# Optimization experiments

Hardware: AMD Instinct MI355X
Metric: run time of the kernel (lower is better)

Reference implementation:

```python
import jax, jax.numpy as jnp
import numpy as np

NUM_CLASSES = 80
L_BOX, L_OBJ, L_CLS = 5.0, 1.0, 1.0


def setup_inputs() -> dict:
    key = jax.random.key(0)
    k0, k1, k2, k3, k4 = jax.random.split(key, 5)
    B, N = 32, 50
    C = 5 + NUM_CLASSES
    pred0 = jax.random.normal(k0, (B, C, 64, 64), dtype=jnp.float32)
    pred1 = jax.random.normal(k1, (B, C, 32, 32), dtype=jnp.float32)
    pred2 = jax.random.normal(k2, (B, C, 16, 16), dtype=jnp.float32)
    # normalized cxcywh in (0,1)
    boxes = jax.random.uniform(k3, (B, N, 4), dtype=jnp.float32, minval=0.01, maxval=0.99)
    labels = jax.random.randint(k4, (B, N), 0, NUM_CLASSES, dtype=jnp.int32)
    return {"pred0": pred0, "pred1": pred1, "pred2": pred2, "boxes": boxes, "labels": labels}


def _bce_with_logits_mean(x, t):
    # numerically stable BCEWithLogits, mean reduction
    return jnp.mean(jnp.maximum(x, 0.0) - x * t + jnp.log1p(jnp.exp(-jnp.abs(x))))


def _build_targets(boxes, labels, b, h, w):
    # boxes: [B,N,4] normalized cxcywh; labels: [B,N]
    B, N, _ = boxes.shape
    bi = jnp.repeat(jnp.arange(B), N)            # [B*N]
    bf = boxes.reshape(-1, 4)                    # [B*N,4]
    lf = labels.reshape(-1)                      # [B*N]
    gx = bf[:, 0] * w
    gy = bf[:, 1] * h
    gi = jnp.minimum(gx.astype(jnp.int32), w - 1)  # int() truncation; gx >= 0
    gj = jnp.minimum(gy.astype(jnp.int32), h - 1)
    obj_t = jnp.zeros((b, 1, h, w), jnp.float32).at[bi, 0, gj, gi].set(1.0)
    vals = jnp.stack([gx - gi, gy - gj, bf[:, 2], bf[:, 3]], axis=1)  # [B*N,4]
    ch4 = jnp.arange(4)
    box_t = jnp.zeros((b, 4, h, w), jnp.float32).at[
        bi[:, None], ch4[None, :], gj[:, None], gi[:, None]].set(vals)
    cls_t = jnp.zeros((b, NUM_CLASSES, h, w), jnp.float32).at[bi, lf, gj, gi].set(1.0)
    return box_t, obj_t, cls_t


def _scale_loss(pred, boxes, labels):
    b, _, h, w = pred.shape
    box_t, obj_t, cls_t = _build_targets(boxes, labels, b, h, w)
    pb = jnp.clip(pred[:, :4], -10.0, 10.0)
    po = jnp.clip(pred[:, 4:5], -10.0, 10.0)
    pc = jnp.clip(pred[:, 5:], -10.0, 10.0)
    box_loss = jnp.mean((pb - box_t) ** 2)
    obj_loss = _bce_with_logits_mean(po, obj_t)
    cls_loss = _bce_with_logits_mean(pc, cls_t)
    # torch code zeroes non-finite losses; clamped logits keep these finite,
    # mirrored with jnp.where for faithfulness
    box_loss = jnp.where(jnp.isfinite(box_loss), box_loss, 0.0)
    obj_loss = jnp.where(jnp.isfinite(obj_loss), obj_loss, 0.0)
    cls_loss = jnp.where(jnp.isfinite(cls_loss), cls_loss, 0.0)
    return L_BOX * box_loss + L_OBJ * obj_loss + L_CLS * cls_loss


def reference(pred0, pred1, pred2, boxes, labels):
    total = (_scale_loss(pred0, boxes, labels)
             + _scale_loss(pred1, boxes, labels)
             + _scale_loss(pred2, boxes, labels))
    return jnp.clip(total / 3.0, 0.0, 1000000.0)
```

## Files before the change

kernel.cpp:

```cpp
#include <hip/hip_runtime.h>
#include <math.h>

#define NCLS 80
#define BB   32
#define NBOX 50
#define CC   85

#define GRID1 2048
#define BLK1  256

__device__ __forceinline__ float clip10(float x) {
    return fminf(fmaxf(x, -10.f), 10.f);
}

__device__ __forceinline__ float bce0(float x) {
    return fmaxf(x, 0.f) + __logf(1.f + __expf(-fabsf(x)));
}

__global__ __launch_bounds__(BLK1) void base_kernel(
    const float* __restrict__ p0, const float* __restrict__ p1,
    const float* __restrict__ p2,
    const float* __restrict__ boxes, const int* __restrict__ labels,
    double* __restrict__ partial)
{
    const int tid = blockIdx.x * BLK1 + threadIdx.x;
    const int nth = GRID1 * BLK1;
    const float* ps[3] = {p0, p1, p2};
    const int hw4s[3]  = {64*64/4, 32*32/4, 16*16/4};

    float part[9];
    #pragma unroll
    for (int s = 0; s < 3; ++s) {
        const float4* p = (const float4*)ps[s];
        const int hw4 = hw4s[s];
        const int n4  = BB * CC * hw4;
        float bx = 0.f, ob = 0.f, cl = 0.f;
        for (int i = tid; i < n4; i += nth) {
            float4 v = p[i];
            int c = (i / hw4) % CC;
            float a0 = clip10(v.x), a1 = clip10(v.y);
            float a2 = clip10(v.z), a3 = clip10(v.w);
            if (c < 4) {
                bx += a0*a0 + a1*a1 + a2*a2 + a3*a3;
            } else if (c == 4) {
                ob += bce0(a0) + bce0(a1) + bce0(a2) + bce0(a3);
            } else {
                cl += bce0(a0) + bce0(a1) + bce0(a2) + bce0(a3);
            }
        }
        part[3*s+0] = bx; part[3*s+1] = ob; part[3*s+2] = cl;
    }

    __shared__ int   s_cell[NBOX];
    __shared__ int   s_lab[NBOX];
    __shared__ float s_vx[NBOX], s_vy[NBOX], s_vw[NBOX], s_vh[NBOX];

    const bool doCorr = (blockIdx.x < 3 * BB);
    const int  cs = blockIdx.x / BB;
    const int  cb = blockIdx.x % BB;
    const int  Ws[3] = {64, 32, 16};

    if (doCorr && threadIdx.x < 64) {
        const int n = threadIdx.x;
        const int W = Ws[cs];
        if (n < NBOX) {
            const float* bp = boxes + ((size_t)cb * NBOX + n) * 4;
            float gx = bp[0] * (float)W;
            float gy = bp[1] * (float)W;
            int gi = min((int)gx, W - 1);
            int gj = min((int)gy, W - 1);
            s_cell[n] = gj * W + gi;
            s_lab[n]  = labels[cb * NBOX + n];
            s_vx[n] = gx - (float)gi;
            s_vy[n] = gy - (float)gj;
            s_vw[n] = bp[2];
            s_vh[n] = bp[3];
        }
    }
    __syncthreads();
    if (doCorr && threadIdx.x < 64) {
        const int n = threadIdx.x;
        const int W = Ws[cs], hw = W * W;
        const float* pred = ps[cs];
        float cbx = 0.f, cob = 0.f, ccl = 0.f;
        if (n < NBOX) {
            const int cell = s_cell[n], lab = s_lab[n];
            bool lastCell = true, lastCls = true;
            for (int m = n + 1; m < NBOX; ++m) {
                if (s_cell[m] == cell) {
                    lastCell = false;
                    if (s_lab[m] == lab) lastCls = false;
                }
            }
            const float* pb_base = pred + (size_t)(cb * CC) * hw + cell;
            if (lastCell) {
                float vals[4] = {s_vx[n], s_vy[n], s_vw[n], s_vh[n]};
                #pragma unroll
                for (int c = 0; c < 4; ++c) {
                    float pb = clip10(pb_base[c * hw]);
                    float d  = pb - vals[c];
                    cbx += d * d - pb * pb;
                }
                float po = clip10(pb_base[4 * hw]);
                cob -= po;
            }
            if (lastCls) {
                float pc = clip10(pb_base[(5 + lab) * hw]);
                ccl -= pc;
            }
        }
        #pragma unroll
        for (int off = 32; off > 0; off >>= 1) {
            cbx += __shfl_down(cbx, off);
            cob += __shfl_down(cob, off);
            ccl += __shfl_down(ccl, off);
        }
        if (n == 0) {
            part[3*cs+0] += cbx;
            part[3*cs+1] += cob;
            part[3*cs+2] += ccl;
        }
    }

    #pragma unroll
    for (int k = 0; k < 9; ++k) {
        float v = part[k];
        #pragma unroll
        for (int off = 32; off > 0; off >>= 1) v += __shfl_down(v, off);
        part[k] = v;
    }
    __shared__ float sred[BLK1/64][9];
    const int wave = threadIdx.x >> 6;
    const int lane = threadIdx.x & 63;
    if (lane == 0) {
        #pragma unroll
        for (int k = 0; k < 9; ++k) sred[wave][k] = part[k];
    }
    __syncthreads();
    if (threadIdx.x == 0) {
        double* o = partial + (size_t)blockIdx.x * 9;
        #pragma unroll
        for (int k = 0; k < 9; ++k)
            o[k] = (double)(sred[0][k] + sred[1][k] + sred[2][k] + sred[3][k]);
    }
}

__global__ __launch_bounds__(256) void final_kernel(
    const double* __restrict__ partial, float* __restrict__ out, int nb)
{
    double loc[9];
    #pragma unroll
    for (int k = 0; k < 9; ++k) loc[k] = 0.0;
    for (int i = threadIdx.x; i < nb; i += 256) {
        const double* row = partial + (size_t)i * 9;
        #pragma unroll
        for (int k = 0; k < 9; ++k) loc[k] += row[k];
    }
    #pragma unroll
    for (int k = 0; k < 9; ++k) {
        double v = loc[k];
        #pragma unroll
        for (int off = 32; off > 0; off >>= 1) v += __shfl_down(v, off);
        loc[k] = v;
    }
    __shared__ double sred[4][9];
    const int wave = threadIdx.x >> 6;
    const int lane = threadIdx.x & 63;
    if (lane == 0) {
        #pragma unroll
        for (int k = 0; k < 9; ++k) sred[wave][k] = loc[k];
    }
    __syncthreads();
    if (threadIdx.x == 0) {
        const double hws[3] = {4096.0, 1024.0, 256.0};
        double total = 0.0;
        #pragma unroll
        for (int s = 0; s < 3; ++s) {
            double hw  = hws[s];
            double tb = sred[0][3*s+0] + sred[1][3*s+0] + sred[2][3*s+0] + sred[3][3*s+0];
            double to = sred[0][3*s+1] + sred[1][3*s+1] + sred[2][3*s+1] + sred[3][3*s+1];
            double tc = sred[0][3*s+2] + sred[1][3*s+2] + sred[2][3*s+2] + sred[3][3*s+2];
            double box = tb / (32.0 * 4.0 * hw);
            double ob  = to / (32.0 * hw);
            double cl  = tc / (32.0 * 80.0 * hw);
            total += 5.0 * box + ob + cl;
        }
        total /= 3.0;
        total = fmin(fmax(total, 0.0), 1000000.0);
        out[0] = (float)total;
    }
}

extern "C" void kernel_launch(void* const* d_in, const int* in_sizes, int n_in,
                              void* d_out, int out_size, void* d_ws, size_t ws_size,
                              hipStream_t stream)
{
    const float* p0     = (const float*)d_in[0];
    const float* p1     = (const float*)d_in[1];
    const float* p2     = (const float*)d_in[2];
    const float* boxes  = (const float*)d_in[3];
    const int*   labels = (const int*)d_in[4];
    float* out = (float*)d_out;

    double* partial = (double*)d_ws;

    base_kernel<<<GRID1, BLK1, 0, stream>>>(p0, p1, p2, boxes, labels, partial);
    final_kernel<<<1, 256, 0, stream>>>(partial, out, GRID1);
}
```

Baseline: 102.5 us.

## Fuse partial and final reductions into one cooperative kernel with grid sync

Merges the per-block partial reduction and the single-block final reduction into one cooperative launch that uses a grid-wide sync, so block 0 finishes the sum without a second kernel launch. The grid is halved to 1024 blocks so that all blocks can be co-resident, and the old two-kernel path is kept as a fallback if the cooperative launch fails. The aim is to remove the second launch and its gap. In exchange it adds grid-barrier cost, and the smaller grid could lower memory-level parallelism.

After: 252.6 us. 2.47x slower.

```diff
diff --git a/kernel.cpp b/kernel.cpp
--- a/kernel.cpp
+++ b/kernel.cpp
@@ -1,12 +1,15 @@
 #include <hip/hip_runtime.h>
+#include <hip/hip_cooperative_groups.h>
 #include <math.h>
+
+namespace cg = cooperative_groups;
 
 #define NCLS 80
 #define BB   32
 #define NBOX 50
 #define CC   85
 
-#define GRID1 2048
+#define GRID1 1024
 #define BLK1  256
 
 __device__ __forceinline__ float clip10(float x) {
@@ -17,14 +20,14 @@
     return fmaxf(x, 0.f) + __logf(1.f + __expf(-fabsf(x)));
 }
 
-__global__ __launch_bounds__(BLK1) void base_kernel(
+__device__ __forceinline__ void compute_block_partials(
     const float* __restrict__ p0, const float* __restrict__ p1,
     const float* __restrict__ p2,
     const float* __restrict__ boxes, const int* __restrict__ labels,
-    double* __restrict__ partial)
-{
-    const int tid = blockIdx.x * BLK1 + threadIdx.x;
-    const int nth = GRID1 * BLK1;
+    int bid, int nblocks, double* __restrict__ partial)
+{
+    const int tid = bid * BLK1 + threadIdx.x;
+    const int nth = nblocks * BLK1;
     const float* ps[3] = {p0, p1, p2};
     const int hw4s[3]  = {64*64/4, 32*32/4, 16*16/4};
 
@@ -55,9 +58,9 @@
     __shared__ int   s_lab[NBOX];
     __shared__ float s_vx[NBOX], s_vy[NBOX], s_vw[NBOX], s_vh[NBOX];
 
-    const bool doCorr = (blockIdx.x < 3 * BB);
-    const int  cs = blockIdx.x / BB;
-    const int  cb = blockIdx.x % BB;
+    const bool doCorr = (bid < 3 * BB);
+    const int  cs = bid / BB;
+    const int  cb = bid % BB;
     const int  Ws[3] = {64, 32, 16};
 
     if (doCorr && threadIdx.x < 64) {
@@ -138,20 +141,20 @@
     }
     __syncthreads();
     if (threadIdx.x == 0) {
-        double* o = partial + (size_t)blockIdx.x * 9;
+        double* o = partial + (size_t)bid * 9;
         #pragma unroll
         for (int k = 0; k < 9; ++k)
             o[k] = (double)(sred[0][k] + sred[1][k] + sred[2][k] + sred[3][k]);
     }
 }
 
-__global__ __launch_bounds__(256) void final_kernel(
+__device__ __forceinline__ void finalize_from_partials(
     const double* __restrict__ partial, float* __restrict__ out, int nb)
 {
     double loc[9];
     #pragma unroll
     for (int k = 0; k < 9; ++k) loc[k] = 0.0;
-    for (int i = threadIdx.x; i < nb; i += 256) {
+    for (int i = threadIdx.x; i < nb; i += BLK1) {
         const double* row = partial + (size_t)i * 9;
         #pragma unroll
         for (int k = 0; k < 9; ++k) loc[k] += row[k];
@@ -163,12 +166,12 @@
         for (int off = 32; off > 0; off >>= 1) v += __shfl_down(v, off);
         loc[k] = v;
     }
-    __shared__ double sred[4][9];
+    __shared__ double dred[BLK1/64][9];
     const int wave = threadIdx.x >> 6;
     const int lane = threadIdx.x & 63;
     if (lane == 0) {
         #pragma unroll
-        for (int k = 0; k < 9; ++k) sred[wave][k] = loc[k];
+        for (int k = 0; k < 9; ++k) dred[wave][k] = loc[k];
     }
     __syncthreads();
     if (threadIdx.x == 0) {
@@ -176,19 +179,47 @@
         double total = 0.0;
         #pragma unroll
         for (int s = 0; s < 3; ++s) {
-            double hw  = hws[s];
-            double tb = sred[0][3*s+0] + sred[1][3*s+0] + sred[2][3*s+0] + sred[3][3*s+0];
-            double to = sred[0][3*s+1] + sred[1][3*s+1] + sred[2][3*s+1] + sred[3][3*s+1];
-            double tc = sred[0][3*s+2] + sred[1][3*s+2] + sred[2][3*s+2] + sred[3][3*s+2];
-            double box = tb / (32.0 * 4.0 * hw);
-            double ob  = to / (32.0 * hw);
-            double cl  = tc / (32.0 * 80.0 * hw);
-            total += 5.0 * box + ob + cl;
+            double hw = hws[s];
+            double tb = dred[0][3*s+0] + dred[1][3*s+0] + dred[2][3*s+0] + dred[3][3*s+0];
+            double to = dred[0][3*s+1] + dred[1][3*s+1] + dred[2][3*s+1] + dred[3][3*s+1];
+            double tc = dred[0][3*s+2] + dred[1][3*s+2] + dred[2][3*s+2] + dred[3][3*s+2];
+            total += 5.0 * (tb / (32.0 * 4.0 * hw))
+                   +       (to / (32.0 * hw))
+                   +       (tc / (32.0 * 80.0 * hw));
         }
         total /= 3.0;
         total = fmin(fmax(total, 0.0), 1000000.0);
         out[0] = (float)total;
     }
+}
+
+__global__ __launch_bounds__(BLK1, 4) void fused_kernel(
+    const float* __restrict__ p0, const float* __restrict__ p1,
+    const float* __restrict__ p2,
+    const float* __restrict__ boxes, const int* __restrict__ labels,
+    double* __restrict__ partial, float* __restrict__ out)
+{
+    compute_block_partials(p0, p1, p2, boxes, labels, blockIdx.x, GRID1, partial);
+    __threadfence();
+    cg::this_grid().sync();
+    if (blockIdx.x == 0) {
+        finalize_from_partials(partial, out, GRID1);
+    }
+}
+
+__global__ __launch_bounds__(BLK1) void base_kernel(
+    const float* __restrict__ p0, const float* __restrict__ p1,
+    const float* __restrict__ p2,
+    const float* __restrict__ boxes, const int* __restrict__ labels,
+    double* __restrict__ partial)
+{
+    compute_block_partials(p0, p1, p2, boxes, labels, blockIdx.x, GRID1, partial);
+}
+
+__global__ __launch_bounds__(BLK1) void final_kernel(
+    const double* __restrict__ partial, float* __restrict__ out)
+{
+    finalize_from_partials(partial, out, GRID1);
 }
 
 extern "C" void kernel_launch(void* const* d_in, const int* in_sizes, int n_in,
@@ -204,6 +235,13 @@
 
     double* partial = (double*)d_ws;
 
-    base_kernel<<<GRID1, BLK1, 0, stream>>>(p0, p1, p2, boxes, labels, partial);
-    final_kernel<<<1, 256, 0, stream>>>(partial, out, GRID1);
-}
+    void* args[] = { (void*)&p0, (void*)&p1, (void*)&p2,
+                     (void*)&boxes, (void*)&labels,
+                     (void*)&partial, (void*)&out };
+    hipError_t err = hipLaunchCooperativeKernel(
+        (const void*)fused_kernel, dim3(GRID1), dim3(BLK1), args, 0, stream);
+    if (err != hipSuccess) {
+        base_kernel<<<GRID1, BLK1, 0, stream>>>(p0, p1, p2, boxes, labels, partial);
+        final_kernel<<<1, BLK1, 0, stream>>>(partial, out);
+    }
+}
```
